# Optimization experiments

Hardware: AMD Instinct MI355X
Metric: run time of the kernel (lower is better)

Reference implementation:

```python
import jax, jax.numpy as jnp
import numpy as np
import math

BS, S, D = 1, 2048, 1024
H = 16
DK = D // H  # 64


def _log_sparse_neighbor_mask(seq_len):
    """mask[i,j]=True iff j==i, or j in [i-k, i) with k=seq_len//2, or i-j is a power of 2.
    Matches generate_log_sparse_plus_neighbors_mask(seq_len, seq_len//2)."""
    k = seq_len // 2
    i = jnp.arange(seq_len, dtype=jnp.int32)[:, None]
    j = jnp.arange(seq_len, dtype=jnp.int32)[None, :]
    diff = i - j
    neighbor = (diff >= 0) & (diff <= k)  # includes diagonal (diff==0)
    pow2 = (diff > 0) & ((diff & (diff - 1)) == 0)
    return neighbor | pow2  # [seq_len, seq_len] bool


def setup_inputs() -> dict:
    key = jax.random.key(0)
    ks = jax.random.split(key, 9)
    std = 0.02
    return {
        "Q": jax.random.normal(ks[0], (BS, S, D), dtype=jnp.float32),
        "Wq": jax.random.normal(ks[1], (D, H * DK), dtype=jnp.float32) * std,
        "bq": jnp.zeros((H * DK,), dtype=jnp.float32),
        "Wk": jax.random.normal(ks[2], (D, H * DK), dtype=jnp.float32) * std,
        "bk": jnp.zeros((H * DK,), dtype=jnp.float32),
        "Wv": jax.random.normal(ks[3], (D, H * DK), dtype=jnp.float32) * std,
        "bv": jnp.zeros((H * DK,), dtype=jnp.float32),
        "Wo": jax.random.normal(ks[4], (H * DK, D), dtype=jnp.float32) * std,
        "bo": jnp.zeros((D,), dtype=jnp.float32),
    }


def reference(Q, Wq, bq, Wk, bk, Wv, bv, Wo, bo):
    bs, s, d = Q.shape
    # QKV projections -> [bs, h, s, dk]
    q = (Q @ Wq + bq).reshape(bs, s, H, DK).transpose(0, 2, 1, 3)
    k = (Q @ Wk + bk).reshape(bs, s, H, DK).transpose(0, 2, 1, 3)
    v = (Q @ Wv + bv).reshape(bs, s, H, DK).transpose(0, 2, 1, 3)

    # log_sparse_attention: scale is 1/sqrt(d_k); mask regenerated internally
    mask = _log_sparse_neighbor_mask(s)  # [s, s] bool
    scores = jnp.einsum("bhqd,bhkd->bhqk", q, k) / math.sqrt(DK)
    scores = jnp.where(mask[None, None, :, :], scores, -jnp.inf)
    attn = jax.nn.softmax(scores, axis=-1)  # [bs, h, s, s]
    out = jnp.einsum("bhqk,bhkd->bhqd", attn, v)

    # merge heads + output projection
    out = out.transpose(0, 2, 1, 3).reshape(bs, s, H * DK)
    out = out @ Wo + bo
    return (out, attn)
```

## Files before the change

kernel.cpp:

```cpp
#include <hip/hip_runtime.h>

#define SEQ 2048
#define DM 1024
#define NH 16
#define DKH 64
#define BAND 1024
#define QKV 3072
#define PBW 1064

typedef __attribute__((ext_vector_type(8))) __bf16 bf16x8;
typedef __attribute__((ext_vector_type(4))) __bf16 bf16x4;
typedef __attribute__((ext_vector_type(4))) float f32x4;

static __device__ __forceinline__ f32x4 mfma16(bf16x8 a, bf16x8 b, f32x4 c) {
  return __builtin_amdgcn_mfma_f32_16x16x32_bf16(a, b, c, 0, 0, 0);
}

#define GLOAD16(gp, lp)                                                        \
  __builtin_amdgcn_global_load_lds(                                            \
      (const __attribute__((address_space(1))) void*)(gp),                     \
      (__attribute__((address_space(3))) void*)(lp), 16, 0, 0)

struct PrepArgs {
  const float* win[4];
  __bf16* wout[4];
  const float* Q;
  __bf16* Qb;
};
__global__ void prep(PrepArgs P) {
  int z = blockIdx.z;
  if (z < 4) {
    __shared__ float t[32][33];
    const float* in = P.win[z];
    __bf16* out = P.wout[z];
    int c0 = blockIdx.x * 32, r0 = blockIdx.y * 32;
    int tx = threadIdx.x, ty = threadIdx.y;
    for (int r = ty; r < 32; r += 8)
      t[r][tx] = in[(size_t)(r0 + r) * DM + c0 + tx];
    __syncthreads();
    for (int r = ty; r < 32; r += 8)
      out[(size_t)(c0 + r) * DM + r0 + tx] = (__bf16)t[tx][r];
  } else {
    int t = threadIdx.y * 32 + threadIdx.x;
    int base = (blockIdx.y * 32 + blockIdx.x) * 512 + t;
#pragma unroll
    for (int u = 0; u < 2; u++) {
      int i = base + u * 256;
      float4 v = reinterpret_cast<const float4*>(P.Q)[i];
      bf16x4 o = {(__bf16)v.x, (__bf16)v.y, (__bf16)v.z, (__bf16)v.w};
      reinterpret_cast<bf16x4*>(P.Qb)[i] = o;
    }
  }
}

template <int BM, int BN, bool BF16OUT, bool VOUT>
__global__ __launch_bounds__(256) void gemm_lds(
    const __bf16* __restrict__ A, const __bf16* __restrict__ BT,
    const float* __restrict__ b0, const float* __restrict__ b1,
    const float* __restrict__ b2, float* __restrict__ Cf,
    __bf16* __restrict__ Cb, __bf16* __restrict__ VT, int M, int N, int K) {
  constexpr int BK = 32;
  constexpr int FM = BM / 32;
  constexpr int FN = BN / 32;
  __shared__ __bf16 lA[2][BM * BK];
  __shared__ __bf16 lB[2][BN * BK];
  int tid = threadIdx.x;
  int lane = tid & 63;
  int l15 = lane & 15, lg = lane >> 4;
  int w = tid >> 6;
  int nwg = gridDim.x * gridDim.y;
  int bid = blockIdx.y * gridDim.x + blockIdx.x;
  int swz = (bid & 7) * (nwg >> 3) + (bid >> 3);
  int bx = swz % gridDim.x;
  int by = swz / gridDim.x;
  int row0 = by * BM;
  int col0 = bx * BN;
  int sec = col0 >> 10;
  const float* bias = sec == 0 ? b0 : (sec == 1 ? b1 : b2);
  int cbase = col0 & (DM - 1);
  int wr = (w >> 1) * (BM / 2);
  int wc = (w & 1) * (BN / 2);
  f32x4 acc[FM][FN] = {};
  const __bf16* aSrc = A + ((size_t)row0 + (tid >> 2)) * K + (tid & 3) * 8;
  const __bf16* bSrc = BT + ((size_t)col0 + (tid >> 2)) * K + (tid & 3) * 8;

  auto stage = [&](int b, int kk) {
#pragma unroll
    for (int s = 0; s < BM / 64; s++)
      GLOAD16(aSrc + (size_t)s * 64 * K + kk, (char*)lA[b] + tid * 16 + s * 4096);
#pragma unroll
    for (int s = 0; s < BN / 64; s++)
      GLOAD16(bSrc + (size_t)s * 64 * K + kk, (char*)lB[b] + tid * 16 + s * 4096);
  };

  stage(0, 0);
  __syncthreads();
  int cur = 0;
  for (int kk = 0; kk < K; kk += BK) {
    if (kk + BK < K) stage(cur ^ 1, kk + BK);
    bf16x8 af[FM], bfr[FN];
#pragma unroll
    for (int mi = 0; mi < FM; mi++)
      af[mi] = *(const bf16x8*)&lA[cur][(wr + mi * 16 + l15) * BK + lg * 8];
#pragma unroll
    for (int ni = 0; ni < FN; ni++)
      bfr[ni] = *(const bf16x8*)&lB[cur][(wc + ni * 16 + l15) * BK + lg * 8];
#pragma unroll
    for (int mi = 0; mi < FM; mi++)
#pragma unroll
      for (int ni = 0; ni < FN; ni++)
        acc[mi][ni] = mfma16(af[mi], bfr[ni], acc[mi][ni]);
    __syncthreads();
    cur ^= 1;
  }
  if (VOUT && sec == 2) {
#pragma unroll
    for (int mi = 0; mi < FM; mi++) {
      int row = row0 + wr + mi * 16 + lg * 4;
#pragma unroll
      for (int ni = 0; ni < FN; ni++) {
        int hd = cbase + wc + ni * 16 + l15;
        float b = bias[hd];
        bf16x4 pk;
#pragma unroll
        for (int r = 0; r < 4; r++) pk[r] = (__bf16)(acc[mi][ni][r] + b);
        *(bf16x4*)&VT[(size_t)hd * SEQ + row] = pk;
      }
    }
    return;
  }
#pragma unroll
  for (int mi = 0; mi < FM; mi++) {
    int row = row0 + wr + mi * 16 + lg * 4;
#pragma unroll
    for (int ni = 0; ni < FN; ni++) {
      int col = col0 + wc + ni * 16 + l15;
      float b = bias[(cbase + wc + ni * 16 + l15) & (DM - 1)];
#pragma unroll
      for (int r = 0; r < 4; r++) {
        float v = acc[mi][ni][r] + b;
        if constexpr (BF16OUT)
          Cb[(size_t)(row + r) * N + col] = (__bf16)v;
        else
          Cf[(size_t)(row + r) * N + col] = v;
      }
    }
  }
}

__global__ __launch_bounds__(256) void attn_fused(
    const __bf16* __restrict__ qkvb, const __bf16* __restrict__ VT,
    float* __restrict__ attn_out, __bf16* __restrict__ pvb) {
  __shared__ __bf16 pbuf[16][PBW];
  __shared__ float wsum[4][16];
  __shared__ float sinv[16];

  int h = blockIdx.y;
  int i0 = blockIdx.x * 16;
  int tid = threadIdx.x, lane = tid & 63, w = tid >> 6;
  int l15 = lane & 15, lg = lane >> 4;

  int jlo = i0 - BAND;
  if (jlo < 0) jlo = 0;
  int ntiles = (i0 + 16 - jlo) >> 4;
  int ktiles = (ntiles + 1) & ~1;
  int n = ntiles * 16;

  const __bf16* qptr = qkvb + (size_t)(i0 + l15) * QKV + h * DKH + lg * 8;
  bf16x8 aq0 = *(const bf16x8*)qptr;
  bf16x8 aq1 = *(const bf16x8*)(qptr + 32);
  const __bf16* kbase = qkvb + DM + h * DKH + lg * 8;

  float sm[4] = {0.f, 0.f, 0.f, 0.f};
  for (int t = w; t < ntiles; t += 4) {
    int jb = jlo + t * 16;
    const __bf16* kptr = kbase + (size_t)(jb + l15) * QKV;
    f32x4 acc = {0.f, 0.f, 0.f, 0.f};
    acc = mfma16(aq0, *(const bf16x8*)kptr, acc);
    acc = mfma16(aq1, *(const bf16x8*)(kptr + 32), acc);
    int col = jb + l15;
    int x = jb - jlo + l15;
#pragma unroll
    for (int r = 0; r < 4; r++) {
      int i = i0 + lg * 4 + r;
      float e = 0.f;
      if (col <= i && i - col <= BAND) {
        e = __expf(acc[r] * 0.125f);
        sm[r] += e;
      }
      pbuf[lg * 4 + r][x] = (__bf16)e;
    }
  }
  if (ktiles != ntiles) pbuf[tid >> 4][n + (tid & 15)] = (__bf16)0.f;
#pragma unroll
  for (int o = 1; o < 16; o <<= 1)
#pragma unroll
    for (int r = 0; r < 4; r++) sm[r] += __shfl_xor(sm[r], o);
  if (l15 == 0)
#pragma unroll
    for (int r = 0; r < 4; r++) wsum[w][lg * 4 + r] = sm[r];
  __syncthreads();
  if (tid < 16)
    sinv[tid] = 1.f / (wsum[0][tid] + wsum[1][tid] + wsum[2][tid] + wsum[3][tid]);
  __syncthreads();

  f32x4 acc = {0.f, 0.f, 0.f, 0.f};
  int d0 = w * 16;
  const __bf16* vtp = VT + ((size_t)h * DKH + d0 + l15) * SEQ;
  for (int kt = 0; kt < ktiles; kt += 2) {
    int kk = kt * 16;
    bf16x8 pa = *(const bf16x8*)&pbuf[l15][kk + lg * 8];
    int jj = jlo + kk + lg * 8;
    bf16x8 vf = {};
    if (jj < SEQ) vf = *(const bf16x8*)(vtp + jj);
    acc = mfma16(pa, vf, acc);
  }
#pragma unroll
  for (int r = 0; r < 4; r++) {
    int row = lg * 4 + r;
    float inv = sinv[row];
    pvb[(size_t)(i0 + row) * DM + h * DKH + d0 + l15] = (__bf16)(acc[r] * inv);
  }

  float* arow = attn_out + ((size_t)h * SEQ + i0) * SEQ;
  int jl4 = jlo >> 2;
  int jh4 = (jlo + n) >> 2;
  f32x4 z = {0.f, 0.f, 0.f, 0.f};
  for (int row = 0; row < 16; row++) {
    f32x4* a4 = (f32x4*)(arow + (size_t)row * SEQ);
    float inv = sinv[row];
    for (int j4 = tid; j4 < jl4; j4 += 256)
      __builtin_nontemporal_store(z, a4 + j4);
    for (int j4 = jl4 + tid; j4 < jh4; j4 += 256) {
      bf16x4 v4 = *(const bf16x4*)&pbuf[row][j4 * 4 - jlo];
      f32x4 o = {(float)v4[0] * inv, (float)v4[1] * inv, (float)v4[2] * inv,
                 (float)v4[3] * inv};
      __builtin_nontemporal_store(o, a4 + j4);
    }
    for (int j4 = jh4 + tid; j4 < SEQ / 4; j4 += 256)
      __builtin_nontemporal_store(z, a4 + j4);
  }
}

extern "C" void kernel_launch(void* const* d_in, const int* in_sizes, int n_in,
                              void* d_out, int out_size, void* d_ws,
                              size_t ws_size, hipStream_t stream) {
  const float* Q = (const float*)d_in[0];
  const float* Wq = (const float*)d_in[1];
  const float* bq = (const float*)d_in[2];
  const float* Wk = (const float*)d_in[3];
  const float* bk = (const float*)d_in[4];
  const float* Wv = (const float*)d_in[5];
  const float* bv = (const float*)d_in[6];
  const float* Wo = (const float*)d_in[7];
  const float* bo = (const float*)d_in[8];
  float* out_proj = (float*)d_out;
  float* attn_out = out_proj + (size_t)SEQ * DM;

  char* ws = (char*)d_ws;
  size_t off = 0;
  auto alloc = [&](size_t bytes) {
    void* p = ws + off;
    off = (off + bytes + 255) & ~(size_t)255;
    return p;
  };
  __bf16* Qb    = (__bf16*)alloc((size_t)SEQ * DM * 2);
  __bf16* WqkvT = (__bf16*)alloc((size_t)QKV * DM * 2);
  __bf16* WoT   = (__bf16*)alloc((size_t)DM * DM * 2);
  __bf16* qkvb  = (__bf16*)alloc((size_t)SEQ * QKV * 2);
  __bf16* VT    = (__bf16*)alloc((size_t)NH * DKH * SEQ * 2);
  __bf16* pvb   = (__bf16*)alloc((size_t)SEQ * DM * 2);

  PrepArgs P;
  P.win[0] = Wq; P.win[1] = Wk; P.win[2] = Wv; P.win[3] = Wo;
  P.wout[0] = WqkvT;
  P.wout[1] = WqkvT + (size_t)DM * DM;
  P.wout[2] = WqkvT + (size_t)2 * DM * DM;
  P.wout[3] = WoT;
  P.Q = Q;
  P.Qb = Qb;
  prep<<<dim3(32, 32, 5), dim3(32, 8), 0, stream>>>(P);

  gemm_lds<128, 128, true, true><<<dim3(QKV / 128, SEQ / 128), 256, 0, stream>>>(
      Qb, WqkvT, bq, bk, bv, nullptr, qkvb, VT, SEQ, QKV, DM);

  attn_fused<<<dim3(SEQ / 16, NH), 256, 0, stream>>>(qkvb, VT, attn_out, pvb);

  gemm_lds<128, 64, false, false><<<dim3(DM / 64, SEQ / 128), 256, 0, stream>>>(
      pvb, WoT, bo, bo, bo, out_proj, nullptr, nullptr, SEQ, DM, DM);
}
```

Baseline: 136.1 us.

## Swizzle attention block order, flatten attn-row stores, shrink GEMM M tiles

The attention kernel now remaps block IDs with an 8-way swizzle, so neighbouring workgroups handle different heads and query tiles. The three-loop zero/value/zero store of the dense attention matrix becomes one flat loop over 16x512 float4 slots that selects between zero and the scaled probability. That store now runs before the PV MFMA loop instead of after it. Both GEMM launches halve the M tile to 64, which doubles the workgroup count for better CU occupancy at the cost of less operand reuse.

Result: faster. 127.1 us (-6.6%).

```diff
diff --git a/kernel.cpp b/kernel.cpp
--- a/kernel.cpp
+++ b/kernel.cpp
@@ -155,8 +155,12 @@
   __shared__ float wsum[4][16];
   __shared__ float sinv[16];
 
-  int h = blockIdx.y;
-  int i0 = blockIdx.x * 16;
+  int nwg = gridDim.x * gridDim.y;
+  int bid = blockIdx.y * gridDim.x + blockIdx.x;
+  int swz = (bid & 7) * (nwg >> 3) + (bid >> 3);
+  int h = swz / (SEQ / 16);
+  int i0 = (swz % (SEQ / 16)) * 16;
+
   int tid = threadIdx.x, lane = tid & 63, w = tid >> 6;
   int l15 = lane & 15, lg = lane >> 4;
 
@@ -203,6 +207,20 @@
   if (tid < 16)
     sinv[tid] = 1.f / (wsum[0][tid] + wsum[1][tid] + wsum[2][tid] + wsum[3][tid]);
   __syncthreads();
+
+  f32x4* abase = (f32x4*)(attn_out + ((size_t)h * SEQ + i0) * SEQ);
+  for (int idx = tid; idx < 16 * (SEQ / 4); idx += 256) {
+    int row = idx >> 9;
+    int j4 = idx & 511;
+    int x = j4 * 4 - jlo;
+    bool valid = (unsigned)x < (unsigned)n;
+    int xc = valid ? x : 0;
+    bf16x4 v4 = *(const bf16x4*)&pbuf[row][xc];
+    float inv = valid ? sinv[row] : 0.f;
+    f32x4 o = {(float)v4[0] * inv, (float)v4[1] * inv, (float)v4[2] * inv,
+               (float)v4[3] * inv};
+    __builtin_nontemporal_store(o, abase + idx);
+  }
 
   f32x4 acc = {0.f, 0.f, 0.f, 0.f};
   int d0 = w * 16;
@@ -220,25 +238,6 @@
     int row = lg * 4 + r;
     float inv = sinv[row];
     pvb[(size_t)(i0 + row) * DM + h * DKH + d0 + l15] = (__bf16)(acc[r] * inv);
-  }
-
-  float* arow = attn_out + ((size_t)h * SEQ + i0) * SEQ;
-  int jl4 = jlo >> 2;
-  int jh4 = (jlo + n) >> 2;
-  f32x4 z = {0.f, 0.f, 0.f, 0.f};
-  for (int row = 0; row < 16; row++) {
-    f32x4* a4 = (f32x4*)(arow + (size_t)row * SEQ);
-    float inv = sinv[row];
-    for (int j4 = tid; j4 < jl4; j4 += 256)
-      __builtin_nontemporal_store(z, a4 + j4);
-    for (int j4 = jl4 + tid; j4 < jh4; j4 += 256) {
-      bf16x4 v4 = *(const bf16x4*)&pbuf[row][j4 * 4 - jlo];
-      f32x4 o = {(float)v4[0] * inv, (float)v4[1] * inv, (float)v4[2] * inv,
-                 (float)v4[3] * inv};
-      __builtin_nontemporal_store(o, a4 + j4);
-    }
-    for (int j4 = jh4 + tid; j4 < SEQ / 4; j4 += 256)
-      __builtin_nontemporal_store(z, a4 + j4);
   }
 }
 
@@ -281,11 +280,11 @@
   P.Qb = Qb;
   prep<<<dim3(32, 32, 5), dim3(32, 8), 0, stream>>>(P);
 
-  gemm_lds<128, 128, true, true><<<dim3(QKV / 128, SEQ / 128), 256, 0, stream>>>(
+  gemm_lds<64, 128, true, true><<<dim3(QKV / 128, SEQ / 64), 256, 0, stream>>>(
       Qb, WqkvT, bq, bk, bv, nullptr, qkvb, VT, SEQ, QKV, DM);
 
   attn_fused<<<dim3(SEQ / 16, NH), 256, 0, stream>>>(qkvb, VT, attn_out, pvb);
 
-  gemm_lds<128, 64, false, false><<<dim3(DM / 64, SEQ / 128), 256, 0, stream>>>(
+  gemm_lds<64, 64, false, false><<<dim3(DM / 64, SEQ / 64), 256, 0, stream>>>(
       pvb, WoT, bo, bo, bo, out_proj, nullptr, nullptr, SEQ, DM, DM);
 }
```
